# Kernel tuning notes

Measured on AMD Instinct MI355X. Metric: run time of the kernel, lower is better.

Reference implementation:

```python
import jax, jax.numpy as jnp
import numpy as np

V = 64                 # |Sigma|
IN_DIM = V + 2         # Sigma + '(' + ')'
OUT_DIM = V + 1        # Sigma + <del>/<end>
H = 512
B = 256
SX = 34                # max proto length 32 + 2 boundaries
SY = 34
BIG_NEG = -1000000000.0


def _one_hot_seq(key, S, batch):
    # '(' at pos 0, L random symbols, ')' at pos L+1, zero padding after
    kl, ks = jax.random.split(key)
    lengths = jax.random.randint(kl, (batch,), 4, S - 1)        # L in [4, S-2]
    syms = jax.random.randint(ks, (S, batch), 0, V)
    pos = jnp.arange(S)[:, None]
    tok = jnp.where(pos == 0, V, jnp.where(pos == lengths[None, :] + 1, V + 1, syms))
    oh = jax.nn.one_hot(tok, IN_DIM, dtype=jnp.float32)
    valid = (pos <= lengths[None, :] + 1).astype(jnp.float32)
    return oh * valid[:, :, None]


def setup_inputs() -> dict:
    key = jax.random.key(0)
    ks = jax.random.split(key, 14)

    def p(k, shape, scale):
        return jax.random.uniform(k, shape, jnp.float32, -scale, scale)

    s = 1.0 / float(np.sqrt(H))
    s2 = 1.0 / float(np.sqrt(2 * H))
    return {
        "sources": _one_hot_seq(ks[0], SX, B),
        "targets": _one_hot_seq(ks[1], SY, B),
        # bidirectional prior LSTM (input IN_DIM -> hidden H, fwd + rev)
        "Wih_f": p(ks[2], (4 * H, IN_DIM), s), "Whh_f": p(ks[3], (4 * H, H), s), "b_f": p(ks[4], (4 * H,), s),
        "Wih_r": p(ks[5], (4 * H, IN_DIM), s), "Whh_r": p(ks[6], (4 * H, H), s), "b_r": p(ks[7], (4 * H,), s),
        # modern LSTM (input IN_DIM -> hidden 2H)
        "Wih_m": p(ks[8], (8 * H, IN_DIM), s2), "Whh_m": p(ks[9], (8 * H, 2 * H), s2), "b_m": p(ks[10], (8 * H,), s2),
        # heads: Linear(2H -> OUT_DIM) + LogSoftmax
        "W_sub": p(ks[11], (OUT_DIM, 2 * H), s2), "b_sub": jnp.zeros((OUT_DIM,), jnp.float32),
        "W_ins": p(ks[12], (OUT_DIM, 2 * H), s2), "b_ins": jnp.zeros((OUT_DIM,), jnp.float32),
    }


def _lstm(x, Wih, Whh, b, hid):
    # torch gate order: i, f, g, o
    bsz = x.shape[1]
    def step(carry, xt):
        h, c = carry
        g = xt @ Wih.T + h @ Whh.T + b
        i, f, gg, o = jnp.split(g, 4, axis=-1)
        c = jax.nn.sigmoid(f) * c + jax.nn.sigmoid(i) * jnp.tanh(gg)
        h = jax.nn.sigmoid(o) * jnp.tanh(c)
        return (h, c), h
    init = (jnp.zeros((bsz, hid), x.dtype), jnp.zeros((bsz, hid), x.dtype))
    _, hs = jax.lax.scan(step, init, x)
    return hs  # [S, B, hid]


def _forward(sources, targets, Wih_f, Whh_f, b_f, Wih_r, Whh_r, b_r,
             Wih_m, Whh_m, b_m, W_sub, b_sub, W_ins, b_ins):
    x_fwd = _lstm(sources, Wih_f, Whh_f, b_f, H)
    x_bwd = _lstm(sources[::-1], Wih_r, Whh_r, b_r, H)[::-1]
    x_emb = jnp.concatenate([x_fwd, x_bwd], axis=-1)   # [SX, B, 2H]
    y_emb = _lstm(targets, Wih_m, Whh_m, b_m, 2 * H)    # [SY, B, 2H]

    # head(x_emb[i] + y_emb[j]) decomposes since Linear is affine
    def pair_logprobs(W, bb):
        lx = jnp.einsum('ibh,oh->ibo', x_emb, W)              # [SX, B, O]
        ly = jnp.einsum('jbh,oh->jbo', y_emb, W) + bb         # [SY, B, O]
        return jax.nn.log_softmax(lx[:, None] + ly[None, :], axis=-1)  # [SX, SY, B, O]

    sub_log = pair_logprobs(W_sub, b_sub)
    ins_log = pair_logprobs(W_ins, b_ins)

    # cell (i, j, b) is computed iff x[i] and y[j] are real (non-padding) one-hots, j <= max_cognat_length
    x_any = sources.sum(-1) > 0                                # [SX, B]
    y_any = targets.sum(-1) > 0                                # [SY, B]
    j_ok = jnp.arange(SY) < SY - 1
    valid = x_any[:, None, :] & (y_any & j_ok[:, None])[None, :, :]   # [SX, SY, B]

    end = jnp.where(valid, ins_log[..., V], BIG_NEG)           # insProbs[V_SIZE]
    dlt = jnp.where(valid, sub_log[..., V], BIG_NEG)           # subProbs[V_SIZE]

    y_next = jnp.pad(targets[1:], ((0, 1), (0, 0), (0, 0)))    # y[j+1], [SY, B, IN_DIM]
    ins_ok = valid & (y_next[..., IN_DIM - 1] == 0)[None]      # not bool(y[j+1, V_SIZE+1])
    ins_val = jnp.einsum('ijbv,jbv->ijb', ins_log[..., :V], y_next[..., :V])
    sub_val = jnp.einsum('ijbv,jbv->ijb', sub_log[..., :V], y_next[..., :V])

    # stacked cached probs: [ins, sub, end, del], each [SX, SY, B]
    return jnp.stack([
        jnp.where(ins_ok, ins_val, BIG_NEG),
        jnp.where(ins_ok, sub_val, BIG_NEG),
        end,
        dlt,
    ])


def reference(sources, targets, Wih_f, Whh_f, b_f, Wih_r, Whh_r, b_r,
              Wih_m, Whh_m, b_m, W_sub, b_sub, W_ins, b_ins):
    return _forward(sources, targets, Wih_f, Whh_f, b_f, Wih_r, Whh_r, b_r,
                    Wih_m, Whh_m, b_m, W_sub, b_sub, W_ins, b_ins)
```

## Files before the change

### kernel.cpp

```cpp
#include <hip/hip_runtime.h>

typedef __attribute__((ext_vector_type(4))) float f32x4;
typedef unsigned char u8;
typedef unsigned long long u64t;

#define BIG_NEG -1000000000.0f

static constexpr int B_  = 256;
static constexpr int SX_ = 34;
static constexpr int SY_ = 34;
static constexpr int IND = 66;
static constexpr int OP_ = 80;

__device__ __forceinline__ f32x4 mfma_fp8(long a, long b, f32x4 c) {
  return __builtin_amdgcn_mfma_f32_16x16x32_fp8_fp8(a, b, c, 0, 0, 0);
}
__device__ __forceinline__ float sigm(float x)  { return 1.0f / (1.0f + __expf(-x)); }
__device__ __forceinline__ float tanhx(float x) { return 2.0f * sigm(2.0f * x) - 1.0f; }
template <bool HI>
__device__ __forceinline__ unsigned pk2(float a, float b, unsigned old) {
  return __builtin_amdgcn_cvt_pk_fp8_f32(a, b, (int)old, HI);
}
__device__ __forceinline__ void ast32(unsigned* p, unsigned v) {
  __hip_atomic_store(p, v, __ATOMIC_RELAXED, __HIP_MEMORY_SCOPE_AGENT);
}
__device__ __forceinline__ unsigned ald32(const unsigned* p) {
  return __hip_atomic_load(p, __ATOMIC_RELAXED, __HIP_MEMORY_SCOPE_AGENT);
}

template <int HH, int NS>
__device__ __forceinline__ void run_lstm(
    const u8* __restrict__ w8, const float* __restrict__ E,
    bool revr, u8* __restrict__ hall, int b0, int h0,
    unsigned* __restrict__ dom_flags, int myid,
    u8* __restrict__ alds, u8* __restrict__ hT, const u8* __restrict__ tok_small) {
  const int tid = threadIdx.x;
  const int lane = tid & 63, w = tid >> 6;
  const int lo = lane & 15, q = lane >> 4;
  constexpr int AST2 = HH + 8;
  constexpr int U8C = HH / 8;
  constexpr int USH = (HH == 1024) ? 7 : 6;
  constexpr int NI  = (32 * U8C) / 256;
  constexpr int NK  = HH / 32;
  const int hh = lo & 7;
  const bool hi = (lo >= 8);
  const int hu_e = h0 + w * 8 + hh;

  long breg0[NK], breg1[NK];
  {
    const u8* brow0 = w8 + (size_t)((lo >> 3) * HH + hu_e) * HH + q * 8;
    const u8* brow1 = w8 + (size_t)((2 + (lo >> 3)) * HH + hu_e) * HH + q * 8;
#pragma unroll
    for (int kk = 0; kk < NK; ++kk) {
      breg0[kk] = *(const long*)(brow0 + kk * 32);
      breg1[kk] = *(const long*)(brow1 + kk * 32);
    }
  }
  float creg[4] = {0.f, 0.f, 0.f, 0.f};

  for (int t = 0; t < 34; ++t) {
    f32x4 acc[2][2];
#pragma unroll
    for (int mt = 0; mt < 2; ++mt) {
      acc[mt][0] = (f32x4){0.f, 0.f, 0.f, 0.f};
      acc[mt][1] = (f32x4){0.f, 0.f, 0.f, 0.f};
    }

    if (t > 0) {
      const u8* hsrc = hall + (size_t)t * (256 * HH);
      u64t tmp[NI];
#pragma unroll
      for (int ii = 0; ii < NI; ++ii) {
        int idx = tid + ii * 256;
        tmp[ii] = __hip_atomic_load(
            (const u64t*)(hsrc + (size_t)(b0 + (idx >> USH)) * HH + (idx & (U8C - 1)) * 8),
            __ATOMIC_RELAXED, __HIP_MEMORY_SCOPE_AGENT);
      }
#pragma unroll
      for (int ii = 0; ii < NI; ++ii) {
        int idx = tid + ii * 256;
        *(u64t*)&alds[(idx >> USH) * AST2 + (idx & (U8C - 1)) * 8] = tmp[ii];
      }
      __syncthreads();

      const u8* a0p = alds + lo * AST2 + q * 8;
      const u8* a1p = alds + (16 + lo) * AST2 + q * 8;
#pragma unroll
      for (int kk = 0; kk < NK; ++kk) {
        long a0 = *(const long*)(a0p + kk * 32);
        long a1 = *(const long*)(a1p + kk * 32);
        acc[0][0] = mfma_fp8(a0, breg0[kk], acc[0][0]);
        acc[0][1] = mfma_fp8(a0, breg1[kk], acc[0][1]);
        acc[1][0] = mfma_fp8(a1, breg0[kk], acc[1][0]);
        acc[1][1] = mfma_fp8(a1, breg1[kk], acc[1][1]);
      }
    }

    int tpos = revr ? 33 - t : t;
    const u8* tkp = tok_small + tpos * 32;
#pragma unroll
    for (int mt = 0; mt < 2; ++mt) {
      f32x4 t0 = acc[mt][0], t1 = acc[mt][1];
      f32x4 p0, p1;
#pragma unroll
      for (int c2 = 0; c2 < 4; ++c2) {
        p0[c2] = __shfl_xor(t0[c2], 8, 64);
        p1[c2] = __shfl_xor(t1[c2], 8, 64);
      }
#pragma unroll
      for (int rr = 0; rr < 2; ++rr) {
        int r = (hi ? 2 : 0) + rr;
        float iv = hi ? p0[r] : t0[r];
        float fv = hi ? t0[r] : p0[r];
        float gv = hi ? p1[r] : t1[r];
        float ov = hi ? t1[r] : p1[r];
        int m = mt * 16 + q * 4 + r;
        int v = tkp[m];
        const float* e = E + (size_t)v * (4 * HH) + hu_e;
        iv += e[0]; fv += e[HH]; gv += e[2 * HH]; ov += e[3 * HH];
        float cold = creg[mt * 2 + rr];
        float cn = sigm(fv) * cold + sigm(iv) * tanhx(gv);
        float hn = sigm(ov) * tanhx(cn);
        creg[mt * 2 + rr] = cn;
        hT[m * 32 + w * 8 + hh] = (u8)(pk2<false>(hn, hn, 0) & 0xffu);
      }
    }
    __syncthreads();

    {
      int m = tid >> 3, cc = tid & 7;
      unsigned val = *(const unsigned*)&hT[m * 32 + cc * 4];
      u8* hdst = hall + (size_t)(t + 1) * (256 * HH);
      ast32((unsigned*)(hdst + (size_t)(b0 + m) * HH + h0 + cc * 4), val);
    }

    if (t < 33) {
      __asm__ volatile("s_waitcnt vmcnt(0)" ::: "memory");
      __syncthreads();
      unsigned tgt = (unsigned)(t + 1);
      if (tid == 0) ast32(&dom_flags[myid * 32], tgt);
      if (tid < NS) {
        int spin = 0;
        for (;;) {
          unsigned v = ald32(&dom_flags[tid * 32]);
          if (__ballot(v < tgt) == 0) break;
          __builtin_amdgcn_s_sleep(1);
          if (++spin > (1 << 17)) break;
        }
      }
      __syncthreads();
    }
  }
}

__global__ __launch_bounds__(256, 2) void mega_kernel(
    const float* __restrict__ sources, const float* __restrict__ targets,
    const float* __restrict__ Wih_f, const float* __restrict__ Whh_f, const float* __restrict__ b_f,
    const float* __restrict__ Wih_r, const float* __restrict__ Whh_r, const float* __restrict__ b_r,
    const float* __restrict__ Wih_m, const float* __restrict__ Whh_m, const float* __restrict__ b_m,
    const float* __restrict__ W_sub, const float* __restrict__ b_sub,
    const float* __restrict__ W_ins, const float* __restrict__ b_ins,
    int* __restrict__ tok_x, int* __restrict__ tok_y,
    u8* __restrict__ Wcat, u8* __restrict__ w8_f, u8* __restrict__ w8_r, u8* __restrict__ w8_m,
    float* __restrict__ E_f, float* __restrict__ E_r, float* __restrict__ E_m,
    u8* __restrict__ fwd_all, u8* __restrict__ rev_all, u8* __restrict__ y_all,
    float* __restrict__ lx_sub, float* __restrict__ lx_ins,
    float* __restrict__ ly_sub, float* __restrict__ ly_ins,
    unsigned* __restrict__ flags) {
  __shared__ u8 smem[43520];
  const int blk = blockIdx.x;
  const int tid = threadIdx.x;

  if (blk < 68) {
    int idx = blk * 256 + tid;
    const int half = SX_ * B_;
    const float* base = (idx < half) ? sources : targets;
    int* outp         = (idx < half) ? tok_x : tok_y;
    int k = (idx < half) ? idx : idx - half;
    const float* p = base + (size_t)k * IND;
    int tok = -1;
    for (int v = 0; v < IND; ++v) if (p[v] > 0.5f) tok = v;
    ast32((unsigned*)&outp[k], (unsigned)tok);
  } else if (blk < 228) {
    int widx = (blk - 68) * 256 + tid;
    int row = widx >> 8;
    int wc  = widx & 255;
    int srow = row < 80 ? row : row - 80;
    const float* W = row < 80 ? W_sub : W_ins;
    float f0 = 0.f, f1 = 0.f, f2 = 0.f, f3 = 0.f;
    if (srow < 65) {
      const float* p = W + (size_t)srow * 1024 + wc * 4;
      f0 = p[0]; f1 = p[1]; f2 = p[2]; f3 = p[3];
    }
    unsigned w = pk2<false>(f0, f1, 0);
    w = pk2<true>(f2, f3, w);
    ast32(&((unsigned*)Wcat)[widx], w);
  } else if (blk < 356) {
    float* tile = (float*)smem;
    int tb = blk - 228;
    const float* W; const float* bias; float* E; int H4; int n0;
    if (tb < 32)      { W = Wih_f; bias = b_f; E = E_f; H4 = 2048; n0 = tb * 64; }
    else if (tb < 64) { W = Wih_r; bias = b_r; E = E_r; H4 = 2048; n0 = (tb - 32) * 64; }
    else              { W = Wih_m; bias = b_m; E = E_m; H4 = 4096; n0 = (tb - 64) * 64; }
    const float* s2 = W + (size_t)n0 * IND;
    for (int i = tid; i < 64 * IND; i += 256) {
      int n = i / IND, v = i - n * IND;
      tile[n * 67 + v] = s2[i];
    }
    __syncthreads();
    int lane = tid & 63, w2 = tid >> 6;
    float bl = bias[n0 + lane];
    for (int v = w2; v < 67; v += 4) {
      float val = (v < 66 ? tile[lane * 67 + v] : 0.f) + bl;
      ast32((unsigned*)&E[(size_t)v * H4 + n0 + lane], __float_as_uint(val));
    }
    __syncthreads();
  }
  {
    const int F4 = 2048 * 512 / 4;
    const int M4 = 4096 * 1024 / 4;
    int i = blk * 256 + tid;
    const int stride = 512 * 256;
    for (; i < 2 * F4 + M4; i += stride) {
      const float* s3; unsigned* dst; int k;
      if (i < F4)          { s3 = Whh_f; dst = (unsigned*)w8_f; k = i; }
      else if (i < 2 * F4) { s3 = Whh_r; dst = (unsigned*)w8_r; k = i - F4; }
      else                 { s3 = Whh_m; dst = (unsigned*)w8_m; k = i - 2 * F4; }
      float4 f = ((const float4*)s3)[k];
      unsigned w3 = pk2<false>(f.x, f.y, 0);
      w3 = pk2<true>(f.z, f.w, w3);
      ast32(&dst[k], w3);
    }
  }

  {
    __asm__ volatile("s_waitcnt vmcnt(0)" ::: "memory");
    __syncthreads();
    if (tid == 0) ast32(&flags[blk * 32], 1u);
    if (tid < 64) {
      int spin = 0;
      for (;;) {
        bool bad = false;
        for (int k = tid; k < 512; k += 64)
          if (ald32(&flags[k * 32]) < 1u) { bad = true; break; }
        if (__ballot(bad) == 0) break;
        __builtin_amdgcn_s_sleep(2);
        if (++spin > (1 << 17)) break;
      }
    }
    __syncthreads();
    __asm__ volatile("" ::: "memory");
  }

  int role, c, s;
  {
    const int b = blk;
    if (b < 256)      { role = 2; c = b >> 5; s = b & 31; }
    else if (b < 384) { int l = b - 256; role = 0; c = l >> 4; s = l & 15; }
    else              { int l = b - 384; role = 1; c = l >> 4; s = l & 15; }
  }
  const float* E  = role == 0 ? E_f  : role == 1 ? E_r  : E_m;
  const u8*    w8 = role == 0 ? w8_f : role == 1 ? w8_r : w8_m;
  u8* hall        = role == 0 ? fwd_all : role == 1 ? rev_all : y_all;
  const int* tokg = (role == 2) ? tok_y : tok_x;
  const int b0 = c * 32;
  const int h0 = s * 32;
  const int dom0 = (role == 2) ? c * 32 : (role == 0) ? 256 + c * 16 : 384 + c * 16;
  unsigned* lf = flags + 512 * 32;
  unsigned* dom_flags = lf + dom0 * 32;

  u8* alds = smem;
  u8* hT = smem + 33024;
  u8* tok_small = smem + 34048;

  for (int i = tid; i < 34 * 32; i += 256) {
    int t2 = i >> 5, m = i & 31;
    int tk = tokg[t2 * 256 + b0 + m];
    tok_small[i] = (u8)(tk < 0 ? 66 : tk);
  }
  __syncthreads();

  if (role == 2)
    run_lstm<1024, 32>(w8, E, false, hall, b0, h0, dom_flags, s, alds, hT, tok_small);
  else
    run_lstm<512, 16>(w8, E, role == 1, hall, b0, h0, dom_flags, s, alds, hT, tok_small);

  {
    __asm__ volatile("s_waitcnt vmcnt(0)" ::: "memory");
    __syncthreads();
    if (tid == 0) ast32(&lf[(dom0 + s) * 32], 34u);
    if (tid < 64) {
      int spin = 0;
      for (;;) {
        bool bad = false;
        for (int k = tid; k < 512; k += 64)
          if (ald32(&lf[k * 32]) < 34u) { bad = true; break; }
        if (__ballot(bad) == 0) break;
        __builtin_amdgcn_s_sleep(2);
        if (++spin > (1 << 17)) break;
      }
    }
    __syncthreads();
    __asm__ volatile("" ::: "memory");
  }

  if (blk >= 272) return;
  {
    u8* wq = smem;
    const int lane = tid & 63, wave = tid >> 6;
    const int lo = lane & 15, q = lane >> 4;
    bool yside = (blk >= 136);
    int mb = yside ? blk - 136 : blk;
    int ij = mb >> 2;
    int bbase = (mb & 3) * 64;

    f32x4 acc[10];
#pragma unroll
    for (int nn = 0; nn < 10; ++nn) acc[nn] = (f32x4){0.f,0.f,0.f,0.f};

    for (int qk = 0; qk < 4; ++qk) {
      long aA[8];
      {
        int row = bbase + wave * 16 + lo;
        const u8* ab;
        if (yside)
          ab = y_all + ((size_t)(ij + 1) * 256 + row) * 1024 + qk * 256 + q * 8;
        else if (qk < 2)
          ab = fwd_all + ((size_t)(ij + 1) * 256 + row) * 512 + qk * 256 + q * 8;
        else
          ab = rev_all + ((size_t)(34 - ij) * 256 + row) * 512 + (qk - 2) * 256 + q * 8;
#pragma unroll
        for (int ki = 0; ki < 8; ++ki) aA[ki] = *(const long*)(ab + ki * 32);
      }
      __syncthreads();
      for (int c8 = tid; c8 < 160 * 32; c8 += 256) {
        int row = c8 >> 5, col = (c8 & 31) << 3;
        *(long*)&wq[row * 264 + col] =
            *(const long*)&Wcat[(size_t)row * 1024 + qk * 256 + col];
      }
      __syncthreads();

#pragma unroll
      for (int ki = 0; ki < 8; ++ki) {
#pragma unroll
        for (int nn = 0; nn < 10; ++nn) {
          long bf = *(const long*)&wq[(nn * 16 + lo) * 264 + ki * 32 + q * 8];
          acc[nn] = mfma_fp8(aA[ki], bf, acc[nn]);
        }
      }
    }

#pragma unroll
    for (int nn = 0; nn < 10; ++nn) {
      bool is_sub = (nn < 5);
      int n = (is_sub ? nn : nn - 5) * 16 + lo;
      float bias = 0.0f;
      if (yside && n < 65) bias = is_sub ? b_sub[n] : b_ins[n];
      float* dst = yside ? (is_sub ? ly_sub : ly_ins) : (is_sub ? lx_sub : lx_ins);
#pragma unroll
      for (int r = 0; r < 4; ++r) {
        int b = bbase + wave * 16 + q * 4 + r;
        dst[((size_t)ij * 256 + b) * OP_ + n] = acc[nn][r] + bias;
      }
    }
  }
}

__device__ __forceinline__ void lse_one(const float4* __restrict__ X,
                                        const float* __restrict__ py, int sym,
                                        float& logZ, float& v64, float& vs) {
  float v[68];
  const float4* py4 = (const float4*)py;
#pragma unroll
  for (int q = 0; q < 17; ++q) {
    float4 yb = py4[q];
    v[4 * q + 0] = X[q].x + yb.x;
    v[4 * q + 1] = X[q].y + yb.y;
    v[4 * q + 2] = X[q].z + yb.z;
    v[4 * q + 3] = X[q].w + yb.w;
  }
  float m = v[0];
#pragma unroll
  for (int o = 1; o < 65; ++o) m = fmaxf(m, v[o]);
  float s = 0.0f, vsl = 0.0f;
#pragma unroll
  for (int o = 0; o < 65; ++o) {
    s += __expf(v[o] - m);
    if (o < 64) vsl = (o == sym) ? v[o] : vsl;
  }
  logZ = m + __logf(s);
  v64 = v[64];
  vs = vsl;
}

__global__ __launch_bounds__(256, 1) void pair_kernel(
    const int* __restrict__ tok_x, const int* __restrict__ tok_y,
    const float* __restrict__ lx_sub, const float* __restrict__ lx_ins,
    const float* __restrict__ ly_sub, const float* __restrict__ ly_ins,
    float* __restrict__ out) {
  const int hsel = blockIdx.x >= 136;
  const int rem = hsel ? blockIdx.x - 136 : blockIdx.x;
  const int i = rem >> 2;
  const int bc = rem & 3;
  const int jq = threadIdx.x >> 6;
  const int bl = threadIdx.x & 63;
  const int b = bc * 64 + bl;
  const size_t CH = (size_t)SX_ * SY_ * B_;
  const float* lx = hsel ? lx_ins : lx_sub;
  const float* ly = hsel ? ly_ins : ly_sub;
  float* outA = out + (hsel ? 0 : CH);
  float* outB = out + (hsel ? 2 * CH : 3 * CH);

  float4 X[17];
  {
    const float4* ps = (const float4*)(lx + ((size_t)i * 256 + b) * OP_);
#pragma unroll
    for (int q = 0; q < 17; ++q) X[q] = ps[q];
  }
  int tx = tok_x[i * 256 + b];

  for (int j = jq; j < 34; j += 4) {
    size_t obase = ((size_t)i * SY_ + j) * 256 + b;
    bool dead = (j == SY_ - 1) || (tx < 0);
    if (!dead) {
      int ty = tok_y[j * 256 + b];
      if (ty < 0) dead = true;
    }
    if (dead) {
      outA[obase] = BIG_NEG;
      outB[obase] = BIG_NEG;
      continue;
    }
    int tn = tok_y[(j + 1) * 256 + b];
    bool ins_ok = (tn != 65);
    int sym = (tn >= 0 && tn < 64) ? tn : -1;

    float logZ, v64, vs;
    lse_one(X, ly + ((size_t)j * 256 + b) * OP_, sym, logZ, v64, vs);
    float valB = v64 - logZ;
    float valA = (sym >= 0) ? (vs - logZ) : 0.0f;
    outA[obase] = ins_ok ? valA : BIG_NEG;
    outB[obase] = valB;
  }
}

extern "C" void kernel_launch(void* const* d_in, const int* in_sizes, int n_in,
                              void* d_out, int out_size, void* d_ws, size_t ws_size,
                              hipStream_t stream) {
  const float* sources = (const float*)d_in[0];
  const float* targets = (const float*)d_in[1];
  const float* Wih_f = (const float*)d_in[2];
  const float* Whh_f = (const float*)d_in[3];
  const float* b_f   = (const float*)d_in[4];
  const float* Wih_r = (const float*)d_in[5];
  const float* Whh_r = (const float*)d_in[6];
  const float* b_r   = (const float*)d_in[7];
  const float* Wih_m = (const float*)d_in[8];
  const float* Whh_m = (const float*)d_in[9];
  const float* b_m   = (const float*)d_in[10];
  const float* W_sub = (const float*)d_in[11];
  const float* b_sub = (const float*)d_in[12];
  const float* W_ins = (const float*)d_in[13];
  const float* b_ins = (const float*)d_in[14];
  float* out = (float*)d_out;

  char* w = (char*)d_ws;
  constexpr size_t FLAG_SZ = 1024 * 32 * 4;
  constexpr size_t TOK_SZ  = (size_t)SX_ * B_ * 4;
  constexpr size_t WCAT_SZ = (size_t)160 * 1024;
  constexpr size_t W8F_SZ  = (size_t)2048 * 512;
  constexpr size_t W8M_SZ  = (size_t)4096 * 1024;
  constexpr size_t EF_SZ   = (size_t)67 * 2048 * 4;
  constexpr size_t EM_SZ   = (size_t)67 * 4096 * 4;
  constexpr size_t LX_SZ   = (size_t)SX_ * B_ * OP_ * 4;
  constexpr size_t HF_SZ   = (size_t)35 * B_ * 512;
  constexpr size_t HM_SZ   = (size_t)35 * B_ * 1024;

  size_t off = 0;
  unsigned* flags = (unsigned*)(w + off); off += FLAG_SZ;
  int*  tok_x   = (int*)(w + off);  off += TOK_SZ;
  int*  tok_y   = (int*)(w + off);  off += TOK_SZ;
  off = (off + 255) & ~(size_t)255;
  u8*   Wcat    = (u8*)(w + off);   off += WCAT_SZ;
  u8*   w8_f    = (u8*)(w + off);   off += W8F_SZ;
  u8*   w8_r    = (u8*)(w + off);   off += W8F_SZ;
  u8*   w8_m    = (u8*)(w + off);   off += W8M_SZ;
  float* E_f    = (float*)(w + off); off += EF_SZ;
  float* E_r    = (float*)(w + off); off += EF_SZ;
  float* E_m    = (float*)(w + off); off += EM_SZ;
  float* lx_sub = (float*)(w + off); off += LX_SZ;
  float* lx_ins = (float*)(w + off); off += LX_SZ;
  float* ly_sub = (float*)(w + off); off += LX_SZ;
  float* ly_ins = (float*)(w + off); off += LX_SZ;
  u8* fwd_all   = (u8*)(w + off);   off += HF_SZ;
  u8* rev_all   = (u8*)(w + off);   off += HF_SZ;
  u8* y_all     = (u8*)(w + off);   off += HM_SZ;
  (void)ws_size; (void)in_sizes; (void)n_in; (void)out_size;

  (void)hipMemsetAsync(flags, 0, FLAG_SZ, stream);

  mega_kernel<<<512, 256, 0, stream>>>(
      sources, targets,
      Wih_f, Whh_f, b_f,
      Wih_r, Whh_r, b_r,
      Wih_m, Whh_m, b_m,
      W_sub, b_sub, W_ins, b_ins,
      tok_x, tok_y,
      Wcat, w8_f, w8_r, w8_m,
      E_f, E_r, E_m,
      fwd_all, rev_all, y_all,
      lx_sub, lx_ins, ly_sub, ly_ins,
      flags);

  pair_kernel<<<272, 256, 0, stream>>>(tok_x, tok_y, lx_sub, lx_ins,
                                       ly_sub, ly_ins, out);
}
```

Baseline: 347.9 us.

## Fuse pair log-softmax stage into mega kernel behind a grid-wide flag barrier

Removes the separate pair_kernel launch and runs the log-softmax pair stage inside the persistent mega kernel. A grid-wide flag barrier is placed after the head projections, and the pair work is split across all 512 blocks by also dividing the j range in half. The loop is rewritten to be branch-free with vectorized loads of Y and fused max/exp reductions. This saves a kernel launch and uses more blocks, but adds a spin barrier and raises register pressure under launch_bounds(256,2).

```diff
diff --git a/kernel.cpp b/kernel.cpp
--- a/kernel.cpp
+++ b/kernel.cpp
@@ -166,7 +166,7 @@
     u8* __restrict__ fwd_all, u8* __restrict__ rev_all, u8* __restrict__ y_all,
     float* __restrict__ lx_sub, float* __restrict__ lx_ins,
     float* __restrict__ ly_sub, float* __restrict__ ly_ins,
-    unsigned* __restrict__ flags) {
+    float* __restrict__ out, unsigned* __restrict__ flags) {
   __shared__ u8 smem[43520];
   const int blk = blockIdx.x;
   const int tid = threadIdx.x;
@@ -304,8 +304,7 @@
     __asm__ volatile("" ::: "memory");
   }
 
-  if (blk >= 272) return;
-  {
+  if (blk < 272) {
     u8* wq = smem;
     const int lane = tid & 63, wave = tid >> 6;
     const int lo = lane & 15, q = lane >> 4;
@@ -360,87 +359,101 @@
 #pragma unroll
       for (int r = 0; r < 4; ++r) {
         int b = bbase + wave * 16 + q * 4 + r;
-        dst[((size_t)ij * 256 + b) * OP_ + n] = acc[nn][r] + bias;
-      }
-    }
-  }
-}
-
-__device__ __forceinline__ void lse_one(const float4* __restrict__ X,
-                                        const float* __restrict__ py, int sym,
-                                        float& logZ, float& v64, float& vs) {
-  float v[68];
-  const float4* py4 = (const float4*)py;
-#pragma unroll
-  for (int q = 0; q < 17; ++q) {
-    float4 yb = py4[q];
-    v[4 * q + 0] = X[q].x + yb.x;
-    v[4 * q + 1] = X[q].y + yb.y;
-    v[4 * q + 2] = X[q].z + yb.z;
-    v[4 * q + 3] = X[q].w + yb.w;
-  }
-  float m = v[0];
-#pragma unroll
-  for (int o = 1; o < 65; ++o) m = fmaxf(m, v[o]);
-  float s = 0.0f, vsl = 0.0f;
-#pragma unroll
-  for (int o = 0; o < 65; ++o) {
-    s += __expf(v[o] - m);
-    if (o < 64) vsl = (o == sym) ? v[o] : vsl;
-  }
-  logZ = m + __logf(s);
-  v64 = v[64];
-  vs = vsl;
-}
-
-__global__ __launch_bounds__(256, 1) void pair_kernel(
-    const int* __restrict__ tok_x, const int* __restrict__ tok_y,
-    const float* __restrict__ lx_sub, const float* __restrict__ lx_ins,
-    const float* __restrict__ ly_sub, const float* __restrict__ ly_ins,
-    float* __restrict__ out) {
-  const int hsel = blockIdx.x >= 136;
-  const int rem = hsel ? blockIdx.x - 136 : blockIdx.x;
-  const int i = rem >> 2;
-  const int bc = rem & 3;
-  const int jq = threadIdx.x >> 6;
-  const int bl = threadIdx.x & 63;
-  const int b = bc * 64 + bl;
-  const size_t CH = (size_t)SX_ * SY_ * B_;
-  const float* lx = hsel ? lx_ins : lx_sub;
-  const float* ly = hsel ? ly_ins : ly_sub;
-  float* outA = out + (hsel ? 0 : CH);
-  float* outB = out + (hsel ? 2 * CH : 3 * CH);
-
-  float4 X[17];
-  {
-    const float4* ps = (const float4*)(lx + ((size_t)i * 256 + b) * OP_);
-#pragma unroll
-    for (int q = 0; q < 17; ++q) X[q] = ps[q];
-  }
-  int tx = tok_x[i * 256 + b];
-
-  for (int j = jq; j < 34; j += 4) {
-    size_t obase = ((size_t)i * SY_ + j) * 256 + b;
-    bool dead = (j == SY_ - 1) || (tx < 0);
-    if (!dead) {
-      int ty = tok_y[j * 256 + b];
-      if (ty < 0) dead = true;
-    }
-    if (dead) {
-      outA[obase] = BIG_NEG;
-      outB[obase] = BIG_NEG;
-      continue;
-    }
-    int tn = tok_y[(j + 1) * 256 + b];
-    bool ins_ok = (tn != 65);
-    int sym = (tn >= 0 && tn < 64) ? tn : -1;
-
-    float logZ, v64, vs;
-    lse_one(X, ly + ((size_t)j * 256 + b) * OP_, sym, logZ, v64, vs);
-    float valB = v64 - logZ;
-    float valA = (sym >= 0) ? (vs - logZ) : 0.0f;
-    outA[obase] = ins_ok ? valA : BIG_NEG;
-    outB[obase] = valB;
+        ast32((unsigned*)&dst[((size_t)ij * 256 + b) * OP_ + n],
+              __float_as_uint(acc[nn][r] + bias));
+      }
+    }
+  }
+
+  unsigned* pf = flags + 1024 * 32;
+  {
+    __asm__ volatile("s_waitcnt vmcnt(0)" ::: "memory");
+    __syncthreads();
+    if (tid == 0) ast32(&pf[blk * 32], 1u);
+    if (tid < 64) {
+      int spin = 0;
+      for (;;) {
+        bool bad = false;
+        for (int k = tid; k < 512; k += 64)
+          if (ald32(&pf[k * 32]) < 1u) { bad = true; break; }
+        if (__ballot(bad) == 0) break;
+        __builtin_amdgcn_s_sleep(2);
+        if (++spin > (1 << 17)) break;
+      }
+    }
+    __syncthreads();
+    __asm__ volatile("" ::: "memory");
+  }
+
+  {
+    const size_t CH = (size_t)SX_ * SY_ * B_;
+    const int jq = tid >> 6, bl = tid & 63;
+    for (int u = blk; u < 544; u += 512) {
+      int hsel = (u >= 272);
+      int rem = hsel ? u - 272 : u;
+      int i = rem >> 3;
+      int bc = (rem >> 1) & 3;
+      int jh = rem & 1;
+      int b = bc * 64 + bl;
+      const float* lx = hsel ? lx_ins : lx_sub;
+      const float* ly = hsel ? ly_ins : ly_sub;
+      float* outA = out + (hsel ? 0 : CH);
+      float* outB = out + (hsel ? 2 * CH : 3 * CH);
+
+      float4 X[17];
+      {
+        const float4* ps = (const float4*)(lx + ((size_t)i * 256 + b) * OP_);
+#pragma unroll
+        for (int q2 = 0; q2 < 17; ++q2) X[q2] = ps[q2];
+      }
+      int tx = tok_x[i * 256 + b];
+
+      for (int j = jh * 17 + jq; j < jh * 17 + 17; j += 4) {
+        float4 Y[17];
+        {
+          const float4* py = (const float4*)(ly + ((size_t)j * 256 + b) * OP_);
+#pragma unroll
+          for (int q2 = 0; q2 < 17; ++q2) Y[q2] = py[q2];
+        }
+        int ty = tok_y[j * 256 + b];
+        int jn = (j < 33) ? j + 1 : 33;
+        int tn = tok_y[jn * 256 + b];
+        bool dead = (j == 33) || (tx < 0) || (ty < 0);
+        bool ins_ok = (tn != 65);
+        int sym = (tn >= 0 && tn < 64) ? tn : -1;
+
+        float v64 = X[16].x + Y[16].x;
+        float m = v64;
+#pragma unroll
+        for (int q2 = 0; q2 < 16; ++q2) {
+          m = fmaxf(m, X[q2].x + Y[q2].x);
+          m = fmaxf(m, X[q2].y + Y[q2].y);
+          m = fmaxf(m, X[q2].z + Y[q2].z);
+          m = fmaxf(m, X[q2].w + Y[q2].w);
+        }
+        float ss = 0.f, vsl = 0.f;
+#pragma unroll
+        for (int q2 = 0; q2 < 16; ++q2) {
+          float v0 = X[q2].x + Y[q2].x;
+          float v1 = X[q2].y + Y[q2].y;
+          float v2 = X[q2].z + Y[q2].z;
+          float v3 = X[q2].w + Y[q2].w;
+          ss += __expf(v0 - m) + __expf(v1 - m) + __expf(v2 - m) + __expf(v3 - m);
+          int o = q2 * 4;
+          vsl = (o == sym) ? v0 : vsl;
+          vsl = (o + 1 == sym) ? v1 : vsl;
+          vsl = (o + 2 == sym) ? v2 : vsl;
+          vsl = (o + 3 == sym) ? v3 : vsl;
+        }
+        ss += __expf(v64 - m);
+        float logZ = m + __logf(ss);
+        float valB = v64 - logZ;
+        float valA = (sym >= 0) ? (vsl - logZ) : 0.0f;
+        size_t obase = ((size_t)i * SY_ + j) * 256 + b;
+        outA[obase] = (dead || !ins_ok) ? BIG_NEG : valA;
+        outB[obase] = dead ? BIG_NEG : valB;
+      }
+    }
   }
 }
 
@@ -465,7 +478,7 @@
   float* out = (float*)d_out;
 
   char* w = (char*)d_ws;
-  constexpr size_t FLAG_SZ = 1024 * 32 * 4;
+  constexpr size_t FLAG_SZ = 1536 * 32 * 4;
   constexpr size_t TOK_SZ  = (size_t)SX_ * B_ * 4;
   constexpr size_t WCAT_SZ = (size_t)160 * 1024;
   constexpr size_t W8F_SZ  = (size_t)2048 * 512;
@@ -510,8 +523,5 @@
       E_f, E_r, E_m,
       fwd_all, rev_all, y_all,
       lx_sub, lx_ins, ly_sub, ly_ins,
-      flags);
-
-  pair_kernel<<<272, 256, 0, stream>>>(tok_x, tok_y, lx_sub, lx_ins,
-                                       ly_sub, ly_ins, out);
-}
+      out, flags);
+}
```

Measured after the change: 346.6 us. About the same (-0.4%).
